# Kernel optimization log

Measured on AMD Instinct MI355X. Metric: run time of the kernel, lower is better.

## Reference

```python
import jax, jax.numpy as jnp
import numpy as np

B, S, D = 2, 2048, 1024
H, DH = 16, 64
LN_EPS = 1e-5
NEG_INF = -1e9


def setup_inputs() -> dict:
    key = jax.random.key(0)
    ks = jax.random.split(key, 8)
    x = jax.random.normal(ks[0], (B, S, D), dtype=jnp.float32)
    mask = jax.random.randint(ks[1], (B, 1, S, S), 0, 5) == 0
    sc = 1.0 / np.sqrt(D)
    W_attn = jax.random.normal(ks[2], (D, 3 * H * DH), dtype=jnp.float32) * sc
    b_attn = jnp.zeros((3 * H * DH,), dtype=jnp.float32)
    W_out = jax.random.normal(ks[3], (H * DH, D), dtype=jnp.float32) * sc
    b_out = jnp.zeros((D,), dtype=jnp.float32)
    ln_g = jnp.ones((D,), dtype=jnp.float32)
    ln_b = jnp.zeros((D,), dtype=jnp.float32)
    return {"x": x, "W_attn": W_attn, "b_attn": b_attn, "W_out": W_out,
            "b_out": b_out, "ln_g": ln_g, "ln_b": ln_b, "mask": mask}


def reference(x, W_attn, b_attn, W_out, b_out, ln_g, ln_b, mask):
    bs, s, _ = x.shape
    qkv = x @ W_attn + b_attn                      # [b, s, 3*H*DH]
    q, k, v = jnp.split(qkv, 3, axis=-1)
    q = q.reshape(bs, s, H, DH)
    k = k.reshape(bs, s, H, DH)
    v = v.reshape(bs, s, H, DH)
    scores = jnp.einsum('bqhd,bkhd->bhqk', q, k) / np.sqrt(DH)
    scores = jnp.where(mask, NEG_INF, scores)
    probs = jax.nn.softmax(scores, axis=-1)        # attn_p = 0 -> dropout is identity
    attn = jnp.einsum('bhqk,bkhd->bqhd', probs, v).reshape(bs, s, H * DH)
    y = x + (attn @ W_out + b_out)                 # resid_p = 0
    mu = jnp.mean(y, axis=-1, keepdims=True)
    var = jnp.mean((y - mu) ** 2, axis=-1, keepdims=True)
    return (y - mu) * jax.lax.rsqrt(var + LN_EPS) * ln_g + ln_b
```

## Files before the change

kernel.cpp:

```cpp
#include <hip/hip_runtime.h>
#include <math.h>

#define BB 2
#define SS 2048
#define DD 1024
#define HH 16
#define DHD 64
#define N3 3072
#define LN_EPS 1e-5f

#define PLANE (BB*HH*SS*DHD)

typedef __attribute__((ext_vector_type(8))) short bf16x8;
typedef __attribute__((ext_vector_type(4))) float f32x4;
typedef unsigned int u32;
typedef unsigned short ushort_t;

static __device__ __forceinline__ short f2bf(float f) {
  union { float f; unsigned u; } a;
  a.f = f;
  unsigned r = a.u + 0x7fffu + ((a.u >> 16) & 1u);
  return (short)(r >> 16);
}

static __device__ __forceinline__ u32 fbits(float f) {
  union { float f; u32 u; } a; a.f = f; return a.u;
}

static __device__ __forceinline__ void gload_lds16(const void* g, void* l) {
  __builtin_amdgcn_global_load_lds(
      (const __attribute__((address_space(1))) u32*)g,
      (__attribute__((address_space(3))) u32*)l, 16, 0, 0);
}

#define PREP_CONV_B   2048
#define PREP_TA_B     768
#define PREP_TO_B     256
#define PREP_PACK_B   32768
#define PREP_TOTAL_B  (PREP_CONV_B + PREP_TA_B + PREP_TO_B + PREP_PACK_B)

__global__ __launch_bounds__(256) void prep_kernel(
    const float* __restrict__ x, ushort_t* __restrict__ xb,
    const float* __restrict__ Wa, ushort_t* __restrict__ watt,
    const float* __restrict__ Wo, ushort_t* __restrict__ wot,
    const int* __restrict__ mask, unsigned long long* __restrict__ bits) {
  __shared__ float tile[64][65];
  const int tid = threadIdx.x;
  const int bid = blockIdx.x;

  if (bid < PREP_CONV_B) {
    int i = (bid * 256 + tid) * 8;
    float4 a = *(const float4*)&x[i];
    float4 b = *(const float4*)&x[i + 4];
    short s[8] = {f2bf(a.x), f2bf(a.y), f2bf(a.z), f2bf(a.w),
                  f2bf(b.x), f2bf(b.y), f2bf(b.z), f2bf(b.w)};
    *(bf16x8*)&xb[i] = *(bf16x8*)s;
    return;
  }
  if (bid < PREP_CONV_B + PREP_TA_B + PREP_TO_B) {
    const float* W; ushort_t* Wt; int K, N, nb, kb;
    if (bid < PREP_CONV_B + PREP_TA_B) {
      int idx = bid - PREP_CONV_B;
      W = Wa; Wt = watt; K = DD; N = N3;
      nb = (idx % 48) * 64; kb = (idx / 48) * 64;
    } else {
      int idx = bid - PREP_CONV_B - PREP_TA_B;
      W = Wo; Wt = wot; K = DD; N = DD;
      nb = (idx % 16) * 64; kb = (idx / 16) * 64;
    }
    #pragma unroll
    for (int i = 0; i < 4; ++i) {
      int idx = tid + i * 256;
      int r = idx >> 4, c = (idx & 15) * 4;
      float4 v = *(const float4*)&W[(size_t)(kb + r) * N + nb + c];
      tile[r][c] = v.x; tile[r][c + 1] = v.y;
      tile[r][c + 2] = v.z; tile[r][c + 3] = v.w;
    }
    __syncthreads();
    #pragma unroll
    for (int i = 0; i < 4; ++i) {
      int idx = tid + i * 256;
      int n = idx >> 4, k = (idx & 15) * 4;
      short4 s;
      s.x = f2bf(tile[k][n]); s.y = f2bf(tile[k + 1][n]);
      s.z = f2bf(tile[k + 2][n]); s.w = f2bf(tile[k + 3][n]);
      *(short4*)&Wt[(size_t)(nb + n) * K + kb + k] = s;
    }
    return;
  }
  {
    size_t g = (size_t)(bid - PREP_CONV_B - PREP_TA_B - PREP_TO_B) * 256 + tid;
    int m = mask[g];
    unsigned long long b = __ballot(m != 0);
    if ((tid & 63) == 0) bits[g >> 6] = b;
  }
}

#define GEMM_MAIN(Aptr, Btptr, Kdim)                                          \
  __shared__ ushort_t As[128 * 64];                                           \
  __shared__ ushort_t Bs[128 * 64];                                           \
  const int tid = threadIdx.x;                                                \
  const int wave = tid >> 6, lane = tid & 63;                                 \
  const int lane16 = lane & 15, quad = lane >> 4;                             \
  const int wm = wave & 1, wn = wave >> 1;                                    \
  const int bm = blockIdx.y * 128, bn = blockIdx.x * 128;                     \
  const int srow = lane >> 3;                                                 \
  const int sg = (lane & 7) ^ srow;                                           \
  f32x4 acc[4][4];                                                            \
  _Pragma("unroll") for (int i = 0; i < 4; ++i)                               \
    _Pragma("unroll") for (int j = 0; j < 4; ++j)                             \
      acc[i][j] = (f32x4){0.f, 0.f, 0.f, 0.f};                                \
  const ushort_t* agp[4];                                                     \
  const ushort_t* bgp[4];                                                     \
  _Pragma("unroll") for (int i = 0; i < 4; ++i) {                             \
    int seg = wave * 4 + i;                                                   \
    int r = seg * 8 + srow;                                                   \
    agp[i] = Aptr + (size_t)(bm + r) * Kdim + sg * 8;                         \
    bgp[i] = Btptr + (size_t)(bn + r) * Kdim + sg * 8;                        \
  }                                                                           \
  for (int k0 = 0; k0 < Kdim; k0 += 64) {                                     \
    _Pragma("unroll") for (int i = 0; i < 4; ++i) {                           \
      int seg = wave * 4 + i;                                                 \
      gload_lds16(agp[i] + k0, &As[seg * 512]);                               \
      gload_lds16(bgp[i] + k0, &Bs[seg * 512]);                               \
    }                                                                         \
    __syncthreads();                                                          \
    _Pragma("unroll") for (int ks = 0; ks < 2; ++ks) {                        \
      bf16x8 af[4], bfr[4];                                                   \
      _Pragma("unroll") for (int mt = 0; mt < 4; ++mt) {                      \
        int ra = wm * 64 + mt * 16 + lane16;                                  \
        int kc = ks * 4 + quad;                                               \
        af[mt] = *(const bf16x8*)&As[ra * 64 + ((kc ^ (ra & 7)) * 8)];        \
      }                                                                       \
      _Pragma("unroll") for (int nt = 0; nt < 4; ++nt) {                      \
        int rb = wn * 64 + nt * 16 + lane16;                                  \
        int kc = ks * 4 + quad;                                               \
        bfr[nt] = *(const bf16x8*)&Bs[rb * 64 + ((kc ^ (rb & 7)) * 8)];       \
      }                                                                       \
      _Pragma("unroll") for (int mt = 0; mt < 4; ++mt)                        \
        _Pragma("unroll") for (int nt = 0; nt < 4; ++nt)                      \
          acc[mt][nt] = __builtin_amdgcn_mfma_f32_16x16x32_bf16(              \
              af[mt], bfr[nt], acc[mt][nt], 0, 0, 0);                         \
    }                                                                         \
    __syncthreads();                                                          \
  }

__global__ __launch_bounds__(256) void gemm_qkv_mfma(
    const ushort_t* __restrict__ A, const ushort_t* __restrict__ Bt,
    const float* __restrict__ bias, ushort_t* __restrict__ qkvh) {
  GEMM_MAIN(A, Bt, DD)
  #pragma unroll
  for (int nt = 0; nt < 4; ++nt) {
    int col = bn + wn * 64 + nt * 16 + lane16;
    int which = col >> 10, hcol = col & 1023;
    int head = hcol >> 6, d = hcol & 63;
    float bv = bias[col];
    ushort_t* plane = qkvh + (size_t)which * PLANE;
    #pragma unroll
    for (int mt = 0; mt < 4; ++mt) {
      #pragma unroll
      for (int reg = 0; reg < 4; ++reg) {
        int row = bm + wm * 64 + mt * 16 + quad * 4 + reg;
        int bb = row >> 11, ss = row & (SS - 1);
        plane[((size_t)(bb * HH + head) * SS + ss) * DHD + d] =
            (ushort_t)f2bf(acc[mt][nt][reg] + bv);
      }
    }
  }
}

__global__ __launch_bounds__(256) void gemm_proj_mfma(
    const ushort_t* __restrict__ A, const ushort_t* __restrict__ Bt,
    const float* __restrict__ bias, const float* __restrict__ xres,
    float* __restrict__ Y) {
  GEMM_MAIN(A, Bt, DD)
  #pragma unroll
  for (int nt = 0; nt < 4; ++nt) {
    int col = bn + wn * 64 + nt * 16 + lane16;
    float bv = bias[col];
    #pragma unroll
    for (int mt = 0; mt < 4; ++mt) {
      #pragma unroll
      for (int reg = 0; reg < 4; ++reg) {
        int row = bm + wm * 64 + mt * 16 + quad * 4 + reg;
        Y[(size_t)row * DD + col] =
            acc[mt][nt][reg] + bv + xres[(size_t)row * DD + col];
      }
    }
  }
}

__global__ __launch_bounds__(256) void vtrans_kernel(
    const ushort_t* __restrict__ vh, ushort_t* __restrict__ vt) {
  __shared__ short t[64][80];
  const int tid = threadIdx.x;
  const int bh = blockIdx.x >> 5;
  const int st = blockIdx.x & 31;
  const size_t hb = (size_t)bh * SS * DHD;
  #pragma unroll
  for (int i = 0; i < 2; ++i) {
    int idx = tid + i * 256;
    int r = idx >> 3, ch = idx & 7;
    bf16x8 v = *(const bf16x8*)&vh[hb + (size_t)(st * 64 + r) * DHD + ch * 8];
    *(bf16x8*)&t[r][ch * 8] = v;
  }
  __syncthreads();
  #pragma unroll
  for (int i = 0; i < 2; ++i) {
    int idx = tid + i * 256;
    int d = idx >> 3, ch = idx & 7;
    short s[8];
    #pragma unroll
    for (int j = 0; j < 8; ++j) s[j] = t[ch * 8 + j][d];
    *(bf16x8*)&vt[hb + (size_t)d * SS + st * 64 + ch * 8] = *(bf16x8*)s;
  }
}

__global__ __launch_bounds__(512) void attn_mfma_kernel(
    const ushort_t* __restrict__ qh, const ushort_t* __restrict__ kh,
    const ushort_t* __restrict__ vt, const u32* __restrict__ mbits,
    ushort_t* __restrict__ attn_out) {
  __shared__ __align__(16) ushort_t Ks[2][64 * 64];
  __shared__ __align__(16) ushort_t Vs[2][64 * 64];
  __shared__ __align__(16) short Pt[8][16][76];

  const int tid = threadIdx.x;
  const int wave = tid >> 6, lane = tid & 63;
  const int lane16 = lane & 15, quad = lane >> 4;

  const int bh = blockIdx.x & 31;
  const int qt = blockIdx.x >> 5;
  const int bbi = bh >> 4, hhi = bh & 15;
  const size_t head_base = (size_t)bh * SS * DHD;
  const int q0 = qt * 128 + wave * 16;
  const int qrow_g = q0 + quad * 4;

  bf16x8 qf[2];
  {
    const float kScale = 0.125f * 1.44269504f;
    const ushort_t* qsrc = &qh[head_base + (size_t)(q0 + lane16) * DHD + quad * 8];
    #pragma unroll
    for (int ks = 0; ks < 2; ++ks) {
      bf16x8 r = *(const bf16x8*)&qsrc[ks * 32];
      #pragma unroll
      for (int e = 0; e < 8; ++e) {
        union { u32 u; float f; } c;
        c.u = ((u32)(ushort_t)r[e]) << 16;
        c.f *= kScale;
        r[e] = f2bf(c.f);
      }
      qf[ks] = r;
    }
  }

  bf16x8 onesf;
  #pragma unroll
  for (int e = 0; e < 8; ++e) onesf[e] = (short)0x3F80;

  f32x4 acc[4];
  f32x4 lacc = (f32x4){0.f, 0.f, 0.f, 0.f};
  #pragma unroll
  for (int dt = 0; dt < 4; ++dt) acc[dt] = (f32x4){0.f, 0.f, 0.f, 0.f};

  const u32* mrow = mbits + ((size_t)(bbi * SS) + q0 + lane16) * 64;
  const int shq = quad * 4;

  const int sr = tid >> 3;
  const int sc_ = tid & 7;
  const int scsrc = sc_ ^ (sr & 7);
  const ushort_t* kstage = kh + head_base + (size_t)sr * DHD + scsrc * 8;
  const ushort_t* vstage = vt + head_base + (size_t)sr * SS + scsrc * 8;
  const int sdst = wave * 512;

  const int swz = (lane16 & 7);

  gload_lds16(kstage, &Ks[0][sdst]);
  gload_lds16(vstage, &Vs[0][sdst]);
  uint2 mcur = *(const uint2*)&mrow[0];
  __syncthreads();

  const int NTILES = SS / 64;
  for (int t = 0; t < NTILES; ++t) {
    const int cur = t & 1;
    uint2 mnext = mcur;
    if (t + 1 < NTILES) {
      gload_lds16(kstage + (size_t)(t + 1) * 64 * DHD, &Ks[cur ^ 1][sdst]);
      gload_lds16(vstage + (t + 1) * 64, &Vs[cur ^ 1][sdst]);
      mnext = *(const uint2*)&mrow[(t + 1) * 2];
    }

    f32x4 sc[4];
    #pragma unroll
    for (int nt = 0; nt < 4; ++nt) {
      sc[nt] = (f32x4){0.f, 0.f, 0.f, 0.f};
      #pragma unroll
      for (int ks = 0; ks < 2; ++ks) {
        int rk = nt * 16 + lane16;
        bf16x8 kf = *(const bf16x8*)&Ks[cur][rk * 64 + (((ks * 4 + quad) ^ swz) * 8)];
        sc[nt] = __builtin_amdgcn_mfma_f32_16x16x32_bf16(kf, qf[ks], sc[nt], 0, 0, 0);
      }
    }

    const u32 tl = mcur.x >> shq;
    const u32 th = mcur.y >> shq;
    #pragma unroll
    for (int nt = 0; nt < 4; ++nt) {
      const u32 w = (nt & 2) ? th : tl;
      const u32 base = (nt & 1) ? 0x10000u : 1u;
      float e0 = (w & (base << 0)) ? 0.f : exp2f(sc[nt][0]);
      float e1 = (w & (base << 1)) ? 0.f : exp2f(sc[nt][1]);
      float e2 = (w & (base << 2)) ? 0.f : exp2f(sc[nt][2]);
      float e3 = (w & (base << 3)) ? 0.f : exp2f(sc[nt][3]);
      u32 w0 = __builtin_amdgcn_perm(fbits(e1) + 0x8000u, fbits(e0) + 0x8000u,
                                     0x07060302u);
      u32 w1 = __builtin_amdgcn_perm(fbits(e3) + 0x8000u, fbits(e2) + 0x8000u,
                                     0x07060302u);
      uint2 pw; pw.x = w0; pw.y = w1;
      *(uint2*)&Pt[wave][lane16][nt * 16 + shq] = pw;
    }

    #pragma unroll
    for (int ks = 0; ks < 2; ++ks) {
      bf16x8 pf = *(const bf16x8*)&Pt[wave][lane16][ks * 32 + quad * 8];
      lacc = __builtin_amdgcn_mfma_f32_16x16x32_bf16(pf, onesf, lacc, 0, 0, 0);
      #pragma unroll
      for (int dt = 0; dt < 4; ++dt) {
        int rv = dt * 16 + lane16;
        bf16x8 vf = *(const bf16x8*)&Vs[cur][rv * 64 + (((ks * 4 + quad) ^ swz) * 8)];
        acc[dt] = __builtin_amdgcn_mfma_f32_16x16x32_bf16(pf, vf, acc[dt], 0, 0, 0);
      }
    }

    mcur = mnext;
    __syncthreads();
  }

  #pragma unroll
  for (int reg = 0; reg < 4; ++reg) {
    float inv = 1.0f / lacc[reg];
    ushort_t* orow = &attn_out[((size_t)(bbi * SS) + qrow_g + reg) * DD
                               + hhi * DHD + lane16];
    #pragma unroll
    for (int dt = 0; dt < 4; ++dt)
      orow[dt * 16] = (ushort_t)f2bf(acc[dt][reg] * inv);
  }
}

__global__ __launch_bounds__(256) void ln_kernel(
    float* __restrict__ Y, const float* __restrict__ g,
    const float* __restrict__ bta) {
  const int r = blockIdx.x;
  const int tid = threadIdx.x;
  float4 v = *(const float4*)&Y[(size_t)r * DD + tid * 4];
  float sum = v.x + v.y + v.z + v.w;
  float sq = v.x * v.x + v.y * v.y + v.z * v.z + v.w * v.w;
  #pragma unroll
  for (int off = 32; off; off >>= 1) {
    sum += __shfl_down(sum, off);
    sq += __shfl_down(sq, off);
  }
  __shared__ float ps[4], pq[4];
  __shared__ float mu_s, rs_s;
  const int wave = tid >> 6;
  if ((tid & 63) == 0) { ps[wave] = sum; pq[wave] = sq; }
  __syncthreads();
  if (tid == 0) {
    float s = ps[0] + ps[1] + ps[2] + ps[3];
    float qq = pq[0] + pq[1] + pq[2] + pq[3];
    float mu = s * (1.0f / DD);
    float var = qq * (1.0f / DD) - mu * mu;
    mu_s = mu;
    rs_s = rsqrtf(var + LN_EPS);
  }
  __syncthreads();
  const float mu = mu_s, rs = rs_s;
  float4 g4 = *(const float4*)&g[tid * 4];
  float4 b4 = *(const float4*)&bta[tid * 4];
  float4 ov;
  ov.x = (v.x - mu) * rs * g4.x + b4.x;
  ov.y = (v.y - mu) * rs * g4.y + b4.y;
  ov.z = (v.z - mu) * rs * g4.z + b4.z;
  ov.w = (v.w - mu) * rs * g4.w + b4.w;
  *(float4*)&Y[(size_t)r * DD + tid * 4] = ov;
}

extern "C" void kernel_launch(void* const* d_in, const int* in_sizes, int n_in,
                              void* d_out, int out_size, void* d_ws, size_t ws_size,
                              hipStream_t stream) {
  const float* x      = (const float*)d_in[0];
  const float* W_attn = (const float*)d_in[1];
  const float* b_attn = (const float*)d_in[2];
  const float* W_out  = (const float*)d_in[3];
  const float* b_out  = (const float*)d_in[4];
  const float* ln_g   = (const float*)d_in[5];
  const float* ln_b   = (const float*)d_in[6];
  const int*   mask   = (const int*)d_in[7];
  float* out = (float*)d_out;
  ushort_t* ws = (ushort_t*)d_ws;

  ushort_t* xb    = ws;
  ushort_t* watt  = xb + (size_t)BB * SS * DD;
  ushort_t* wot   = watt + (size_t)N3 * DD;
  ushort_t* qh    = wot + (size_t)DD * DD;
  ushort_t* kh    = qh + (size_t)PLANE;
  ushort_t* vh    = kh + (size_t)PLANE;
  ushort_t* attnb = vh + (size_t)PLANE;
  u32* mbits      = (u32*)(attnb + (size_t)BB * SS * DD);
  ushort_t* vtb   = xb;

  prep_kernel<<<dim3(PREP_TOTAL_B), 256, 0, stream>>>(
      x, xb, W_attn, watt, W_out, wot, mask, (unsigned long long*)mbits);

  gemm_qkv_mfma<<<dim3(N3 / 128, (BB * SS) / 128), 256, 0, stream>>>(
      xb, watt, b_attn, qh);
  vtrans_kernel<<<dim3(BB * HH * (SS / 64)), 256, 0, stream>>>(vh, vtb);
  attn_mfma_kernel<<<dim3(BB * HH * (SS / 128)), 512, 0, stream>>>(
      qh, kh, vtb, mbits, attnb);
  gemm_proj_mfma<<<dim3(DD / 128, (BB * SS) / 128), 256, 0, stream>>>(
      attnb, wot, b_out, x, out);
  ln_kernel<<<dim3(BB * SS), 256, 0, stream>>>(out, ln_g, ln_b);
}
```

Before: 262.7 us.

## Restructure attention to 32x32 MFMA with split-K across waves and register P

The attention kernel switches from 16x16x32 to 32x32x16 bf16 MFMA tiles. Each wave now handles 32 query rows over half of the key sequence, and the two halves are merged through LDS at the end. The P matrix stays in registers, using v_permlane32_swap in place of an LDS round-trip, and the row sum is accumulated with scalar adds instead of a ones-MFMA. This targets LDS traffic and the extra MFMA work, at the cost of more registers, a final cross-wave reduction, and a larger staged shared-memory footprint.

```diff
diff --git a/kernel.cpp b/kernel.cpp
--- a/kernel.cpp
+++ b/kernel.cpp
@@ -13,6 +13,7 @@
 
 typedef __attribute__((ext_vector_type(8))) short bf16x8;
 typedef __attribute__((ext_vector_type(4))) float f32x4;
+typedef __attribute__((ext_vector_type(16))) float f32x16;
 typedef unsigned int u32;
 typedef unsigned short ushort_t;
 
@@ -25,6 +26,17 @@
 
 static __device__ __forceinline__ u32 fbits(float f) {
   union { float f; u32 u; } a; a.f = f; return a.u;
+}
+
+static __device__ __forceinline__ float ex2(float x) {
+  float r;
+  asm("v_exp_f32 %0, %1" : "=v"(r) : "v"(x));
+  return r;
+}
+
+static __device__ __forceinline__ u32 pkbf(float lo, float hi) {
+  return __builtin_amdgcn_perm(fbits(hi) + 0x8000u, fbits(lo) + 0x8000u,
+                               0x07060302u);
 }
 
 static __device__ __forceinline__ void gload_lds16(const void* g, void* l) {
@@ -216,32 +228,31 @@
   }
 }
 
-__global__ __launch_bounds__(512) void attn_mfma_kernel(
+__global__ __launch_bounds__(512, 4) void attn_mfma_kernel(
     const ushort_t* __restrict__ qh, const ushort_t* __restrict__ kh,
     const ushort_t* __restrict__ vt, const u32* __restrict__ mbits,
     ushort_t* __restrict__ attn_out) {
-  __shared__ __align__(16) ushort_t Ks[2][64 * 64];
-  __shared__ __align__(16) ushort_t Vs[2][64 * 64];
-  __shared__ __align__(16) short Pt[8][16][76];
+  __shared__ __align__(16) ushort_t S[2][2][2][4096];
 
   const int tid = threadIdx.x;
   const int wave = tid >> 6, lane = tid & 63;
-  const int lane16 = lane & 15, quad = lane >> 4;
+  const int l31 = lane & 31, hi = lane >> 5;
 
   const int bh = blockIdx.x & 31;
   const int qt = blockIdx.x >> 5;
   const int bbi = bh >> 4, hhi = bh & 15;
   const size_t head_base = (size_t)bh * SS * DHD;
-  const int q0 = qt * 128 + wave * 16;
-  const int qrow_g = q0 + quad * 4;
-
-  bf16x8 qf[2];
+  const int wq = wave & 3, khx = wave >> 2;
+  const int q32 = qt * 128 + wq * 32;
+  const int qrow = q32 + l31;
+
+  bf16x8 qf[4];
   {
     const float kScale = 0.125f * 1.44269504f;
-    const ushort_t* qsrc = &qh[head_base + (size_t)(q0 + lane16) * DHD + quad * 8];
-    #pragma unroll
-    for (int ks = 0; ks < 2; ++ks) {
-      bf16x8 r = *(const bf16x8*)&qsrc[ks * 32];
+    const ushort_t* qsrc = &qh[head_base + (size_t)qrow * DHD + hi * 8];
+    #pragma unroll
+    for (int dk = 0; dk < 4; ++dk) {
+      bf16x8 r = *(const bf16x8*)&qsrc[dk * 16];
       #pragma unroll
       for (int e = 0; e < 8; ++e) {
         union { u32 u; float f; } c;
@@ -249,100 +260,124 @@
         c.f *= kScale;
         r[e] = f2bf(c.f);
       }
-      qf[ks] = r;
-    }
-  }
-
-  bf16x8 onesf;
-  #pragma unroll
-  for (int e = 0; e < 8; ++e) onesf[e] = (short)0x3F80;
-
-  f32x4 acc[4];
-  f32x4 lacc = (f32x4){0.f, 0.f, 0.f, 0.f};
-  #pragma unroll
-  for (int dt = 0; dt < 4; ++dt) acc[dt] = (f32x4){0.f, 0.f, 0.f, 0.f};
-
-  const u32* mrow = mbits + ((size_t)(bbi * SS) + q0 + lane16) * 64;
-  const int shq = quad * 4;
+      qf[dk] = r;
+    }
+  }
+
+  f32x16 acc0, acc1;
+  #pragma unroll
+  for (int e = 0; e < 16; ++e) { acc0[e] = 0.f; acc1[e] = 0.f; }
+  float lsum = 0.f;
+
+  const u32* mrow = mbits + ((size_t)(bbi * SS) + qrow) * 64 + khx * 32;
 
   const int sr = tid >> 3;
-  const int sc_ = tid & 7;
-  const int scsrc = sc_ ^ (sr & 7);
-  const ushort_t* kstage = kh + head_base + (size_t)sr * DHD + scsrc * 8;
-  const ushort_t* vstage = vt + head_base + (size_t)sr * SS + scsrc * 8;
+  const int scsrc = (tid & 7) ^ (sr & 7);
+  const ushort_t* kst0 = kh + head_base + (size_t)sr * DHD + scsrc * 8;
+  const ushort_t* vst0 = vt + head_base + (size_t)sr * SS + scsrc * 8;
   const int sdst = wave * 512;
 
-  const int swz = (lane16 & 7);
-
-  gload_lds16(kstage, &Ks[0][sdst]);
-  gload_lds16(vstage, &Vs[0][sdst]);
-  uint2 mcur = *(const uint2*)&mrow[0];
+#define ATTN_STAGE(buf, t)                                                    \
+  gload_lds16(kst0 + (size_t)(t) * 64 * DHD, &S[buf][0][0][sdst]);            \
+  gload_lds16(kst0 + (size_t)(1024 + (t) * 64) * DHD, &S[buf][0][1][sdst]);   \
+  gload_lds16(vst0 + (t) * 64, &S[buf][1][0][sdst]);                          \
+  gload_lds16(vst0 + 1024 + (t) * 64, &S[buf][1][1][sdst]);
+
+  ATTN_STAGE(0, 0);
+  uint2 mcur = *(const uint2*)mrow;
   __syncthreads();
 
-  const int NTILES = SS / 64;
-  for (int t = 0; t < NTILES; ++t) {
+  const int NT = 16;
+  for (int t = 0; t < NT; ++t) {
     const int cur = t & 1;
     uint2 mnext = mcur;
-    if (t + 1 < NTILES) {
-      gload_lds16(kstage + (size_t)(t + 1) * 64 * DHD, &Ks[cur ^ 1][sdst]);
-      gload_lds16(vstage + (t + 1) * 64, &Vs[cur ^ 1][sdst]);
+    if (t + 1 < NT) {
+      ATTN_STAGE(cur ^ 1, t + 1);
       mnext = *(const uint2*)&mrow[(t + 1) * 2];
     }
 
-    f32x4 sc[4];
-    #pragma unroll
-    for (int nt = 0; nt < 4; ++nt) {
-      sc[nt] = (f32x4){0.f, 0.f, 0.f, 0.f};
-      #pragma unroll
-      for (int ks = 0; ks < 2; ++ks) {
-        int rk = nt * 16 + lane16;
-        bf16x8 kf = *(const bf16x8*)&Ks[cur][rk * 64 + (((ks * 4 + quad) ^ swz) * 8)];
-        sc[nt] = __builtin_amdgcn_mfma_f32_16x16x32_bf16(kf, qf[ks], sc[nt], 0, 0, 0);
-      }
-    }
-
-    const u32 tl = mcur.x >> shq;
-    const u32 th = mcur.y >> shq;
-    #pragma unroll
-    for (int nt = 0; nt < 4; ++nt) {
-      const u32 w = (nt & 2) ? th : tl;
-      const u32 base = (nt & 1) ? 0x10000u : 1u;
-      float e0 = (w & (base << 0)) ? 0.f : exp2f(sc[nt][0]);
-      float e1 = (w & (base << 1)) ? 0.f : exp2f(sc[nt][1]);
-      float e2 = (w & (base << 2)) ? 0.f : exp2f(sc[nt][2]);
-      float e3 = (w & (base << 3)) ? 0.f : exp2f(sc[nt][3]);
-      u32 w0 = __builtin_amdgcn_perm(fbits(e1) + 0x8000u, fbits(e0) + 0x8000u,
-                                     0x07060302u);
-      u32 w1 = __builtin_amdgcn_perm(fbits(e3) + 0x8000u, fbits(e2) + 0x8000u,
-                                     0x07060302u);
-      uint2 pw; pw.x = w0; pw.y = w1;
-      *(uint2*)&Pt[wave][lane16][nt * 16 + shq] = pw;
-    }
-
-    #pragma unroll
-    for (int ks = 0; ks < 2; ++ks) {
-      bf16x8 pf = *(const bf16x8*)&Pt[wave][lane16][ks * 32 + quad * 8];
-      lacc = __builtin_amdgcn_mfma_f32_16x16x32_bf16(pf, onesf, lacc, 0, 0, 0);
-      #pragma unroll
-      for (int dt = 0; dt < 4; ++dt) {
-        int rv = dt * 16 + lane16;
-        bf16x8 vf = *(const bf16x8*)&Vs[cur][rv * 64 + (((ks * 4 + quad) ^ swz) * 8)];
-        acc[dt] = __builtin_amdgcn_mfma_f32_16x16x32_bf16(pf, vf, acc[dt], 0, 0, 0);
+    const ushort_t* Kb = &S[cur][0][khx][0];
+    const ushort_t* Vb = &S[cur][1][khx][0];
+
+    f32x16 s0, s1;
+    #pragma unroll
+    for (int e = 0; e < 16; ++e) { s0[e] = 0.f; s1[e] = 0.f; }
+    #pragma unroll
+    for (int dk = 0; dk < 4; ++dk) {
+      const int c = 2 * dk + hi;
+      const int r0 = l31;
+      bf16x8 kf0 = *(const bf16x8*)&Kb[r0 * 64 + ((c ^ (r0 & 7)) * 8)];
+      s0 = __builtin_amdgcn_mfma_f32_32x32x16_bf16(kf0, qf[dk], s0, 0, 0, 0);
+      const int r1 = 32 + l31;
+      bf16x8 kf1 = *(const bf16x8*)&Kb[r1 * 64 + ((c ^ (r1 & 7)) * 8)];
+      s1 = __builtin_amdgcn_mfma_f32_32x32x16_bf16(kf1, qf[dk], s1, 0, 0, 0);
+    }
+
+    #pragma unroll
+    for (int ks16 = 0; ks16 < 4; ++ks16) {
+      const int ksub = ks16 >> 1;
+      const int g0 = (ks16 & 1) * 2;
+      const f32x16 sv = ksub ? s1 : s0;
+      const u32 w32 = ksub ? mcur.y : mcur.x;
+      const u32 na = w32 >> (g0 * 8 + hi * 4);
+      const u32 nb = w32 >> (g0 * 8 + 8 + hi * 4);
+      float e0 = (na & 1u) ? 0.f : ex2(sv[g0 * 4 + 0]);
+      float e1 = (na & 2u) ? 0.f : ex2(sv[g0 * 4 + 1]);
+      float e2 = (na & 4u) ? 0.f : ex2(sv[g0 * 4 + 2]);
+      float e3 = (na & 8u) ? 0.f : ex2(sv[g0 * 4 + 3]);
+      float f0 = (nb & 1u) ? 0.f : ex2(sv[g0 * 4 + 4]);
+      float f1 = (nb & 2u) ? 0.f : ex2(sv[g0 * 4 + 5]);
+      float f2 = (nb & 4u) ? 0.f : ex2(sv[g0 * 4 + 6]);
+      float f3 = (nb & 8u) ? 0.f : ex2(sv[g0 * 4 + 7]);
+      lsum += ((e0 + e1) + (e2 + e3)) + ((f0 + f1) + (f2 + f3));
+      u32 a0 = pkbf(e0, e1), a1 = pkbf(e2, e3);
+      u32 b0 = pkbf(f0, f1), b1 = pkbf(f2, f3);
+      asm("v_permlane32_swap_b32 %0, %1" : "+v"(a0), "+v"(b0));
+      asm("v_permlane32_swap_b32 %0, %1" : "+v"(a1), "+v"(b1));
+      union { u32 w[4]; bf16x8 v; } pfu;
+      pfu.w[0] = a0; pfu.w[1] = a1; pfu.w[2] = b0; pfu.w[3] = b1;
+      {
+        const int rv0 = l31;
+        const int cv = 2 * ks16 + hi;
+        bf16x8 vf0 = *(const bf16x8*)&Vb[rv0 * 64 + ((cv ^ (rv0 & 7)) * 8)];
+        acc0 = __builtin_amdgcn_mfma_f32_32x32x16_bf16(pfu.v, vf0, acc0, 0, 0, 0);
+        const int rv1 = 32 + l31;
+        bf16x8 vf1 = *(const bf16x8*)&Vb[rv1 * 64 + ((cv ^ (rv1 & 7)) * 8)];
+        acc1 = __builtin_amdgcn_mfma_f32_32x32x16_bf16(pfu.v, vf1, acc1, 0, 0, 0);
       }
     }
 
     mcur = mnext;
     __syncthreads();
   }
-
-  #pragma unroll
-  for (int reg = 0; reg < 4; ++reg) {
-    float inv = 1.0f / lacc[reg];
-    ushort_t* orow = &attn_out[((size_t)(bbi * SS) + qrow_g + reg) * DD
-                               + hhi * DHD + lane16];
-    #pragma unroll
-    for (int dt = 0; dt < 4; ++dt)
-      orow[dt * 16] = (ushort_t)f2bf(acc[dt][reg] * inv);
+#undef ATTN_STAGE
+
+  float* mbuf = (float*)&S[0][0][0][0];
+  float* lbuf = mbuf + 4 * 64 * 32;
+  lbuf[((khx * 4 + wq) * 2 + hi) * 32 + l31] = lsum;
+  if (khx == 1) {
+    float* dst = mbuf + (size_t)(wq * 64 + lane) * 32;
+    #pragma unroll
+    for (int e = 0; e < 16; ++e) { dst[e] = acc0[e]; dst[16 + e] = acc1[e]; }
+  }
+  __syncthreads();
+  if (khx == 0) {
+    const float* src = mbuf + (size_t)(wq * 64 + lane) * 32;
+    #pragma unroll
+    for (int e = 0; e < 16; ++e) { acc0[e] += src[e]; acc1[e] += src[16 + e]; }
+    #pragma unroll
+    for (int reg = 0; reg < 16; ++reg) {
+      const int kq = (reg & 3) + 8 * (reg >> 2) + 4 * hi;
+      float lq = lbuf[((0 * 4 + wq) * 2 + 0) * 32 + kq]
+               + lbuf[((0 * 4 + wq) * 2 + 1) * 32 + kq]
+               + lbuf[((1 * 4 + wq) * 2 + 0) * 32 + kq]
+               + lbuf[((1 * 4 + wq) * 2 + 1) * 32 + kq];
+      const float inv = 1.0f / lq;
+      ushort_t* orow = &attn_out[((size_t)(bbi * SS) + q32 + kq) * DD
+                                 + hhi * DHD];
+      orow[l31] = (ushort_t)f2bf(acc0[reg] * inv);
+      orow[32 + l31] = (ushort_t)f2bf(acc1[reg] * inv);
+    }
   }
 }
 
```

Result: faster. 241.9 us (-7.9%).
